# Optimization experiments

Hardware: AMD Instinct MI355X
Metric: run time of the kernel (lower is better)

Reference implementation:

```python
import jax, jax.numpy as jnp
import numpy as np


def setup_inputs() -> dict:
    key = jax.random.key(0)
    ks = jax.random.split(key, 8)
    B, Tq, S, H = 32, 4, 2048, 1024
    return {
        "query": jax.random.normal(ks[0], (B, Tq, H), dtype=jnp.float32),
        "keys": jax.random.normal(ks[1], (S, B, 2 * H), dtype=jnp.float32),
        "Wa_w": jax.random.normal(ks[2], (H, H), dtype=jnp.float32) * 0.02,
        "Wa_b": jax.random.normal(ks[3], (H,), dtype=jnp.float32) * 0.02,
        "Ua_w": jax.random.normal(ks[4], (H, 2 * H), dtype=jnp.float32) * 0.02,
        "Ua_b": jax.random.normal(ks[5], (H,), dtype=jnp.float32) * 0.02,
        "Va_w": jax.random.normal(ks[6], (1, H), dtype=jnp.float32) * 0.02,
        "Va_b": jax.random.normal(ks[7], (1,), dtype=jnp.float32) * 0.02,
    }


def reference(query, keys, Wa_w, Wa_b, Ua_w, Ua_b, Va_w, Va_b):
    # query: [B, Tq, H] -> last step [B, 1, H]
    q = query[:, -1:, :]
    # keys: [S, B, 2H] -> [B, S, 2H]
    k = jnp.transpose(keys, (1, 0, 2))
    # Additive attention scores: Va(tanh(Wa(q) + Ua(k)))
    wq = q @ Wa_w.T + Wa_b                      # [B, 1, H]
    uk = k @ Ua_w.T + Ua_b                      # [B, S, H]
    scores = jnp.tanh(wq + uk) @ Va_w.T + Va_b  # [B, S, 1]
    scores = jnp.transpose(scores, (0, 2, 1))   # [B, 1, S]
    weights = jax.nn.softmax(scores, axis=-1)   # [B, 1, S]
    context = jnp.einsum('bqs,bsd->bqd', weights, k)  # [B, 1, 2H]
    return (context, weights)
```

## Files before the change

kernel.cpp:

```cpp
#include <hip/hip_runtime.h>
#include <hip/hip_bf16.h>

typedef __attribute__((ext_vector_type(4))) float f32x4;
typedef __attribute__((ext_vector_type(8))) short short8;

#define B_   32
#define S_   2048
#define H_   1024
#define D2_  2048
#define BM   256
#define BN   256
#define BK   64
#define NKT  32
#define TILE_SH 16384


__device__ __forceinline__ short f2bf(float f) {
  unsigned u = __float_as_uint(f);
  u = (u + 0x7fffu + ((u >> 16) & 1u)) >> 16;
  return (short)u;
}

__device__ __forceinline__ float bf2f(short s) {
  return __uint_as_float(((unsigned)(unsigned short)s) << 16);
}

__device__ __forceinline__ short8 cvt8(f32x4 a, f32x4 b) {
  short8 o;
  o[0] = f2bf(a.x); o[1] = f2bf(a.y); o[2] = f2bf(a.z); o[3] = f2bf(a.w);
  o[4] = f2bf(b.x); o[5] = f2bf(b.y); o[6] = f2bf(b.z); o[7] = f2bf(b.w);
  return o;
}

__device__ __forceinline__ float fast_tanh(float x) {
  float e = __builtin_amdgcn_exp2f(x * 2.885390081777927f);
  return 1.0f - 2.0f * __builtin_amdgcn_rcpf(e + 1.0f);
}

__device__ __forceinline__ void gload16(const short* g, short* l) {
  __builtin_amdgcn_global_load_lds((const __attribute__((address_space(1))) void*)g,
                                   (__attribute__((address_space(3))) void*)l, 16, 0, 0);
}

__global__ void k_convert_ua(const float* __restrict__ src, short* __restrict__ dst) {
  int idx = blockIdx.x * 256 + threadIdx.x;
  int wu  = idx & 2047;
  int kt  = (idx >> 11) & 31;
  int nt  = idx >> 16;
  int row = wu >> 3;
  int sl  = wu & 7;
  int q   = sl ^ (row & 7);
  const float* s = src + (size_t)(nt * 256 + row) * D2_ + kt * 64 + q * 8;
  f32x4 a = *(const f32x4*)s;
  f32x4 b = *(const f32x4*)(s + 4);
  *(short8*)(dst + (size_t)idx * 8) = cvt8(a, b);
}

__global__ void k_convert_keys(const float* __restrict__ src, short* __restrict__ dst) {
  int idx = blockIdx.x * 256 + threadIdx.x;
  int wu  = idx & 2047;
  int kt  = (idx >> 11) & 31;
  int mt  = idx >> 16;
  int row = wu >> 3;
  int sl  = wu & 7;
  int q   = sl ^ (row & 7);
  const float* s = src + (size_t)(mt * 256 + row) * D2_ + kt * 64 + q * 8;
  f32x4 a = *(const f32x4*)s;
  f32x4 b = *(const f32x4*)(s + 4);
  *(short8*)(dst + (size_t)idx * 8) = cvt8(a, b);
}

__global__ void k_wq(const float* __restrict__ query, const float* __restrict__ Wa_w,
                     const float* __restrict__ Wa_b, const float* __restrict__ Ua_b,
                     float* __restrict__ wqb) {
  int b = blockIdx.x;
  int hc = blockIdx.y;
  int t = threadIdx.x;
  __shared__ float q[H_];
  for (int i = t; i < H_; i += 256) q[i] = query[(size_t)b * (4 * H_) + 3 * H_ + i];
  __syncthreads();
  int h = hc * 128 + (t >> 1);
  int kh = (t & 1) * 512;
  const float* wr = Wa_w + (size_t)h * H_ + kh;
  float acc = 0.f;
  #pragma unroll 8
  for (int k = 0; k < 512; k += 4) {
    f32x4 wv = *(const f32x4*)(wr + k);
    acc += wv.x * q[kh + k] + wv.y * q[kh + k + 1] + wv.z * q[kh + k + 2] + wv.w * q[kh + k + 3];
  }
  acc += __shfl_xor(acc, 1);
  if ((t & 1) == 0) wqb[b * H_ + h] = acc + Wa_b[h] + Ua_b[h];
}

#define AF_READ(mA, mB)                                         \
  af[0] = *(const short8*)&Ac[aread0 + (mA) * 1024];            \
  af[1] = *(const short8*)&Ac[aread1 + (mA) * 1024];            \
  af[2] = *(const short8*)&Ac[aread0 + (mB) * 1024];            \
  af[3] = *(const short8*)&Ac[aread1 + (mB) * 1024];

#define MFMA16(mA, mB)                                                                            \
  __builtin_amdgcn_s_setprio(1);                                                                  \
  _Pragma("unroll")                                                                               \
  for (int n = 0; n < 4; ++n) {                                                                   \
    acc[mA][n] = __builtin_amdgcn_mfma_f32_16x16x32_bf16(af[0], bf[2*n],   acc[mA][n], 0, 0, 0);  \
    acc[mA][n] = __builtin_amdgcn_mfma_f32_16x16x32_bf16(af[1], bf[2*n+1], acc[mA][n], 0, 0, 0);  \
    acc[mB][n] = __builtin_amdgcn_mfma_f32_16x16x32_bf16(af[2], bf[2*n],   acc[mB][n], 0, 0, 0);  \
    acc[mB][n] = __builtin_amdgcn_mfma_f32_16x16x32_bf16(af[3], bf[2*n+1], acc[mB][n], 0, 0, 0);  \
  }                                                                                               \
  __builtin_amdgcn_s_setprio(0);

#define STAGE4(src_, dst_)                         \
  gload16((src_) + 0 * 4096, (dst_) + 0 * 4096 + wu); \
  gload16((src_) + 1 * 4096, (dst_) + 1 * 4096 + wu); \
  gload16((src_) + 2 * 4096, (dst_) + 2 * 4096 + wu); \
  gload16((src_) + 3 * 4096, (dst_) + 3 * 4096 + wu);

__global__ __launch_bounds__(512, 2) void k_gemm_score(
    const short* __restrict__ keys_bf, const short* __restrict__ uab_t,
    const float* __restrict__ wqb, const float* __restrict__ va,
    float* __restrict__ scores_p) {
  __shared__ short As[2][TILE_SH];
  __shared__ short Bs[2][TILE_SH];

  const int bid = blockIdx.x;
  const int g = (bid & 7) * 128 + (bid >> 3);
  const int mt = g >> 2;
  const int nt = g & 3;
  const int r0 = mt * BM;
  const int h0 = nt * BN;

  const int t = threadIdx.x;
  const int lane = t & 63;
  const int w = t >> 6;
  const int wm = w >> 2;
  const int wn = w & 3;

  f32x4 acc[8][4] = {};

  const short* abase = keys_bf + (size_t)mt * (NKT * TILE_SH) + t * 8;
  const short* bbase = uab_t  + (size_t)nt * (NKT * TILE_SH) + t * 8;
  const int wu = w * 512;

  const int lr = lane & 15;
  const int lq = lane >> 4;
  const int sl0 = lq ^ (lr & 7);
  const int aread0 = (wm * 128 + lr) * 64 + sl0 * 8;
  const int aread1 = aread0 ^ 32;
  const int bread0 = (wn * 64 + lr) * 64 + sl0 * 8;
  const int bread1 = bread0 ^ 32;

  {
    STAGE4(abase, &As[0][0])
    STAGE4(bbase, &Bs[0][0])
    asm volatile("s_waitcnt vmcnt(0)" ::: "memory");
    __builtin_amdgcn_s_barrier();
  }

  #pragma unroll 1
  for (int kt = 0; kt < NKT; ++kt) {
    const int cb = kt & 1;
    const bool stage = (kt < NKT - 1);
    const short* Ac = As[cb];
    const short* Bc = Bs[cb];
    const short* anext = abase + (size_t)(kt + 1) * TILE_SH;
    const short* bnext = bbase + (size_t)(kt + 1) * TILE_SH;
    short* Anb = &As[cb ^ 1][0];
    short* Bnb = &Bs[cb ^ 1][0];
    short8 bf[8], af[4];

    #pragma unroll
    for (int n = 0; n < 4; ++n) {
      bf[2 * n]     = *(const short8*)&Bc[bread0 + n * 1024];
      bf[2 * n + 1] = *(const short8*)&Bc[bread1 + n * 1024];
    }
    AF_READ(0, 1)
    if (stage) { STAGE4(anext, Anb) }
    __builtin_amdgcn_s_barrier();
    asm volatile("s_waitcnt lgkmcnt(0)" ::: "memory");
    MFMA16(0, 1)
    __builtin_amdgcn_s_barrier();

    AF_READ(2, 3)
    if (stage) { STAGE4(bnext, Bnb) }
    __builtin_amdgcn_s_barrier();
    asm volatile("s_waitcnt lgkmcnt(0)" ::: "memory");
    MFMA16(2, 3)
    __builtin_amdgcn_s_barrier();

    AF_READ(4, 5)
    __builtin_amdgcn_s_barrier();
    asm volatile("s_waitcnt lgkmcnt(0)" ::: "memory");
    MFMA16(4, 5)
    __builtin_amdgcn_s_barrier();

    AF_READ(6, 7)
    __builtin_amdgcn_s_barrier();
    asm volatile("s_waitcnt lgkmcnt(0)" ::: "memory");
    MFMA16(6, 7)
    asm volatile("s_waitcnt vmcnt(0)" ::: "memory");
    __builtin_amdgcn_s_barrier();
  }

  const int lgrp = lane >> 4;
  const int lc = lane & 15;
  float vah[4];
  #pragma unroll
  for (int n = 0; n < 4; ++n) vah[n] = va[h0 + wn * 64 + n * 16 + lc];
  #pragma unroll
  for (int m = 0; m < 8; ++m) {
    #pragma unroll
    for (int reg = 0; reg < 4; ++reg) {
      int row = wm * 128 + m * 16 + lgrp * 4 + reg;
      int r = r0 + row;
      int bb = r & (B_ - 1);
      const float* wrow = wqb + bb * H_ + h0 + wn * 64 + lc;
      float s = 0.f;
      #pragma unroll
      for (int n = 0; n < 4; ++n)
        s += vah[n] * fast_tanh(acc[m][n][reg] + wrow[n * 16]);
      s += __shfl_xor(s, 1);
      s += __shfl_xor(s, 2);
      s += __shfl_xor(s, 4);
      s += __shfl_xor(s, 8);
      if (lc == 0) scores_p[(size_t)r * 16 + nt * 4 + wn] = s;
    }
  }
}

__global__ __launch_bounds__(512, 2) void k_gemm_rs(
    const float* __restrict__ keys, const short* __restrict__ uab_t,
    const float* __restrict__ wqb, const float* __restrict__ va,
    float* __restrict__ scores_p) {
  __shared__ short As[2][TILE_SH];
  __shared__ short Bs[2][TILE_SH];
  const int bid = blockIdx.x;
  const int g = (bid & 7) * 128 + (bid >> 3);
  const int mt = g >> 2;
  const int nt = g & 3;
  const int r0 = mt * BM;
  const int h0 = nt * BN;
  const int t = threadIdx.x;
  const int lane = t & 63;
  const int w = t >> 6;
  const int wm = w >> 2;
  const int wn = w & 3;
  f32x4 acc[8][4] = {};
  const int arow = t >> 1;
  const int ahalf = t & 1;
  const float* abase = keys + (size_t)(r0 + arow) * D2_ + ahalf * 32;
  int awoff[4];
  #pragma unroll
  for (int j = 0; j < 4; ++j)
    awoff[j] = arow * 64 + ((((ahalf << 2) | j) ^ (arow & 7)) << 3);
  const short* bbase = uab_t + (size_t)nt * NKT * TILE_SH + t * 8;
  const int wu = w * 512;
  const int lr = lane & 15;
  const int lq = lane >> 4;
  const int sl0 = lq ^ (lr & 7);
  const int aread0 = (wm * 128 + lr) * 64 + sl0 * 8;
  const int aread1 = aread0 ^ 32;
  const int bread0 = (wn * 64 + lr) * 64 + sl0 * 8;
  const int bread1 = bread0 ^ 32;
  {
    f32x4 v[8];
    #pragma unroll
    for (int j = 0; j < 8; ++j) v[j] = *(const f32x4*)(abase + j * 4);
    #pragma unroll
    for (int j = 0; j < 4; ++j)
      *(short8*)&As[0][awoff[j]] = cvt8(v[2 * j], v[2 * j + 1]);
    STAGE4(bbase, &Bs[0][0])
    asm volatile("s_waitcnt vmcnt(0) lgkmcnt(0)" ::: "memory");
    __builtin_amdgcn_s_barrier();
  }
  f32x4 av[8];
  #pragma unroll 1
  for (int kt = 0; kt < NKT; ++kt) {
    const int cb = kt & 1;
    const bool stage = (kt < NKT - 1);
    const float* anext = abase + (kt + 1) * BK;
    const short* bnext = bbase + (size_t)(kt + 1) * TILE_SH;
    short* Bnb = &Bs[cb ^ 1][0];
    const short* Ac = As[cb];
    const short* Bc = Bs[cb];
    short8 bf[8], af[4];
    #pragma unroll
    for (int n = 0; n < 4; ++n) {
      bf[2 * n]     = *(const short8*)&Bc[bread0 + n * 1024];
      bf[2 * n + 1] = *(const short8*)&Bc[bread1 + n * 1024];
    }
    AF_READ(0, 1)
    if (stage) {
      #pragma unroll
      for (int j = 0; j < 8; ++j) av[j] = *(const f32x4*)(anext + j * 4);
    }
    __builtin_amdgcn_s_barrier();
    asm volatile("s_waitcnt lgkmcnt(0)" ::: "memory");
    MFMA16(0, 1)
    __builtin_amdgcn_s_barrier();
    AF_READ(2, 3)
    if (stage) {
      gload16(bnext + 0 * 4096, Bnb + 0 * 4096 + wu);
      gload16(bnext + 1 * 4096, Bnb + 1 * 4096 + wu);
    }
    __builtin_amdgcn_s_barrier();
    asm volatile("s_waitcnt lgkmcnt(0)" ::: "memory");
    MFMA16(2, 3)
    __builtin_amdgcn_s_barrier();
    AF_READ(4, 5)
    if (stage) {
      gload16(bnext + 2 * 4096, Bnb + 2 * 4096 + wu);
      gload16(bnext + 3 * 4096, Bnb + 3 * 4096 + wu);
    }
    __builtin_amdgcn_s_barrier();
    asm volatile("s_waitcnt lgkmcnt(0)" ::: "memory");
    MFMA16(4, 5)
    __builtin_amdgcn_s_barrier();
    AF_READ(6, 7)
    if (stage) {
      #pragma unroll
      for (int j = 0; j < 4; ++j)
        *(short8*)&As[cb ^ 1][awoff[j]] = cvt8(av[2 * j], av[2 * j + 1]);
    }
    __builtin_amdgcn_s_barrier();
    asm volatile("s_waitcnt lgkmcnt(0)" ::: "memory");
    MFMA16(6, 7)
    asm volatile("s_waitcnt vmcnt(0) lgkmcnt(0)" ::: "memory");
    __builtin_amdgcn_s_barrier();
  }
  const int lgrp = lane >> 4;
  const int lc = lane & 15;
  float vah[4];
  #pragma unroll
  for (int n = 0; n < 4; ++n) vah[n] = va[h0 + wn * 64 + n * 16 + lc];
  #pragma unroll
  for (int m = 0; m < 8; ++m) {
    #pragma unroll
    for (int reg = 0; reg < 4; ++reg) {
      int row = wm * 128 + m * 16 + lgrp * 4 + reg;
      int r = r0 + row;
      int bb = r & (B_ - 1);
      const float* wrow = wqb + bb * H_ + h0 + wn * 64 + lc;
      float s = 0.f;
      #pragma unroll
      for (int n = 0; n < 4; ++n)
        s += vah[n] * fast_tanh(acc[m][n][reg] + wrow[n * 16]);
      s += __shfl_xor(s, 1);
      s += __shfl_xor(s, 2);
      s += __shfl_xor(s, 4);
      s += __shfl_xor(s, 8);
      if (lc == 0) scores_p[(size_t)r * 16 + nt * 4 + wn] = s;
    }
  }
}

__global__ void k_softmax(const float* __restrict__ scores_p, float* __restrict__ out) {
  int b = blockIdx.x;
  int t = threadIdx.x;
  __shared__ float sc[S_];
  __shared__ float red[4];
  float lmax = -3.4e38f;
  #pragma unroll
  for (int i = 0; i < 8; ++i) {
    int s = t + i * 256;
    const float* p = scores_p + ((size_t)s * B_ + b) * 16;
    f32x4 p0 = *(const f32x4*)p;
    f32x4 p1 = *(const f32x4*)(p + 4);
    f32x4 p2 = *(const f32x4*)(p + 8);
    f32x4 p3 = *(const f32x4*)(p + 12);
    f32x4 ps = p0 + p1 + p2 + p3;
    float v = ps.x + ps.y + ps.z + ps.w;
    sc[s] = v;
    lmax = fmaxf(lmax, v);
  }
  #pragma unroll
  for (int o = 32; o >= 1; o >>= 1) lmax = fmaxf(lmax, __shfl_xor(lmax, o));
  if ((t & 63) == 0) red[t >> 6] = lmax;
  __syncthreads();
  float gmax = fmaxf(fmaxf(red[0], red[1]), fmaxf(red[2], red[3]));
  __syncthreads();
  float lsum = 0.f;
  #pragma unroll
  for (int i = 0; i < 8; ++i) {
    int s = t + i * 256;
    float e = __builtin_amdgcn_exp2f((sc[s] - gmax) * 1.4426950408889634f);
    sc[s] = e;
    lsum += e;
  }
  #pragma unroll
  for (int o = 32; o >= 1; o >>= 1) lsum += __shfl_xor(lsum, o);
  if ((t & 63) == 0) red[t >> 6] = lsum;
  __syncthreads();
  float inv = 1.0f / (red[0] + red[1] + red[2] + red[3]);
  for (int i = 0; i < 8; ++i) {
    int s = t + i * 256;
    out[(size_t)65536 + b * S_ + s] = sc[s] * inv;
  }
}

__global__ __launch_bounds__(256) void k_ctx_partial_bf2(const short* __restrict__ keys_bf,
                                                         const float* __restrict__ wts,
                                                         float* __restrict__ cp) {
  const int kt = blockIdx.x;
  const int mtc = blockIdx.y;
  const int t = threadIdx.x;
  const int cg = t >> 5;
  const int b = t & 31;
  const int slot = cg ^ (b & 7);
  const float* wbase = wts + (size_t)b * S_ + mtc * 128;
  f32x4 accA = {}, accB = {};
  #pragma unroll 2
  for (int c = 0; c < 16; ++c) {
    const short* tb = keys_bf + ((size_t)((mtc * 16 + c) * 32 + kt)) * TILE_SH + (slot << 3);
    f32x4 w0 = *(const f32x4*)(wbase + c * 8);
    f32x4 w1 = *(const f32x4*)(wbase + c * 8 + 4);
    float wg[8] = {w0.x, w0.y, w0.z, w0.w, w1.x, w1.y, w1.z, w1.w};
    #pragma unroll
    for (int s8 = 0; s8 < 8; ++s8) {
      short8 v = *(const short8*)(tb + (s8 * 32 + b) * 64);
      float wgt = wg[s8];
      accA.x += wgt * bf2f(v[0]); accA.y += wgt * bf2f(v[1]);
      accA.z += wgt * bf2f(v[2]); accA.w += wgt * bf2f(v[3]);
      accB.x += wgt * bf2f(v[4]); accB.y += wgt * bf2f(v[5]);
      accB.z += wgt * bf2f(v[6]); accB.w += wgt * bf2f(v[7]);
    }
  }
  float* o = cp + ((size_t)mtc * B_ + b) * D2_ + kt * 64 + cg * 8;
  *(f32x4*)o = accA;
  *(f32x4*)(o + 4) = accB;
}

__global__ void k_ctx_partial(const float* __restrict__ keys, const float* __restrict__ wts,
                              float* __restrict__ cp) {
  int b = blockIdx.x;
  int dc = blockIdx.y;
  int scn = blockIdx.z;
  int t = threadIdx.x;
  __shared__ float wl[256];
  int s0 = scn * 256;
  wl[t] = wts[b * S_ + s0 + t];
  __syncthreads();
  int d = dc * 1024 + t * 4;
  f32x4 acc = {};
  #pragma unroll 4
  for (int i = 0; i < 256; ++i) {
    int s = s0 + i;
    f32x4 kv = *(const f32x4*)(keys + ((size_t)s * B_ + b) * D2_ + d);
    acc += kv * wl[i];
  }
  *(f32x4*)(cp + ((size_t)scn * B_ + b) * D2_ + d) = acc;
}

__global__ void k_ctx_reduce(const float* __restrict__ cp, float* __restrict__ out, int np) {
  int i = blockIdx.x * 256 + threadIdx.x;
  float s = 0.f;
  for (int j = 0; j < np; ++j) s += cp[(size_t)j * 65536 + i];
  out[i] = s;
}

extern "C" void kernel_launch(void* const* d_in, const int* in_sizes, int n_in,
                              void* d_out, int out_size, void* d_ws, size_t ws_size,
                              hipStream_t stream) {
  const float* query = (const float*)d_in[0];
  const float* keys  = (const float*)d_in[1];
  const float* Wa_w  = (const float*)d_in[2];
  const float* Wa_b  = (const float*)d_in[3];
  const float* Ua_w  = (const float*)d_in[4];
  const float* Ua_b  = (const float*)d_in[5];
  const float* Va_w  = (const float*)d_in[6];
  float* out = (float*)d_out;
  char* ws = (char*)d_ws;

  const size_t KEYS_BF_BYTES = 268435456ull;
  const size_t TAIL = 16ull * 1024 * 1024;
  bool big = ws_size >= KEYS_BF_BYTES + TAIL;

  if (big) {
    short* keys_bf = (short*)ws;
    char* base = ws + KEYS_BF_BYTES;
    short* uab_t = (short*)(base);
    float* wqb = (float*)(base + 4u * 1024 * 1024);
    float* sp  = (float*)(base + 4u * 1024 * 1024 + 128 * 1024);
    float* cp  = (float*)(base + 8u * 1024 * 1024 + 256 * 1024);

    hipLaunchKernelGGL(k_convert_ua, dim3(1024), dim3(256), 0, stream, Ua_w, uab_t);
    hipLaunchKernelGGL(k_convert_keys, dim3(65536), dim3(256), 0, stream, keys, keys_bf);
    hipLaunchKernelGGL(k_wq, dim3(32, 8), dim3(256), 0, stream, query, Wa_w, Wa_b, Ua_b, wqb);
    hipLaunchKernelGGL(k_gemm_score, dim3(1024), dim3(512), 0, stream, keys_bf, uab_t, wqb, Va_w, sp);
    hipLaunchKernelGGL(k_softmax, dim3(32), dim3(256), 0, stream, sp, out);
    hipLaunchKernelGGL(k_ctx_partial_bf2, dim3(32, 16), dim3(256), 0, stream, keys_bf, out + 65536, cp);
    hipLaunchKernelGGL(k_ctx_reduce, dim3(256), dim3(256), 0, stream, cp, out, 16);
  } else {
    short* uab_t = (short*)(ws);
    float* wqb = (float*)(ws + 4u * 1024 * 1024);
    float* sp  = (float*)(ws + 4u * 1024 * 1024 + 128 * 1024);
    float* cp  = (float*)(ws + 8u * 1024 * 1024 + 256 * 1024);

    hipLaunchKernelGGL(k_convert_ua, dim3(1024), dim3(256), 0, stream, Ua_w, uab_t);
    hipLaunchKernelGGL(k_wq, dim3(32, 8), dim3(256), 0, stream, query, Wa_w, Wa_b, Ua_b, wqb);
    hipLaunchKernelGGL(k_gemm_rs, dim3(1024), dim3(512), 0, stream, keys, uab_t, wqb, Va_w, sp);
    hipLaunchKernelGGL(k_softmax, dim3(32), dim3(256), 0, stream, sp, out);
    hipLaunchKernelGGL(k_ctx_partial, dim3(32, 2, 8), dim3(256), 0, stream, keys, out + 65536, cp);
    hipLaunchKernelGGL(k_ctx_reduce, dim3(256), dim3(256), 0, stream, cp, out, 8);
  }
}
```

Baseline: 507.8 us.

## Halve GEMM K-tile to 32 and cut per-iteration barriers in score kernels

Shrinks the GEMM K tile from 64 to 32, doubling the K iterations. The pre-swizzled bf16 layouts in the convert kernels and the context kernel are rewritten to match the new 32-wide tiles. The main loop now loads all A/B fragments up front and uses partial lgkmcnt waits with sched_barrier, issuing MFMAs in two groups and replacing about eight barriers per iteration with one or two. The aim is to cut synchronization overhead and shared-memory footprint, possibly raising occupancy. The cost is more loop iterations, with less MFMA work available to hide global-load latency in each one.

```diff
diff --git a/kernel.cpp b/kernel.cpp
--- a/kernel.cpp
+++ b/kernel.cpp
@@ -10,9 +10,9 @@
 #define D2_  2048
 #define BM   256
 #define BN   256
-#define BK   64
-#define NKT  32
-#define TILE_SH 16384
+#define BK   32
+#define NKT  64
+#define TILE_SH 8192
 
 
 __device__ __forceinline__ short f2bf(float f) {
@@ -44,13 +44,13 @@
 
 __global__ void k_convert_ua(const float* __restrict__ src, short* __restrict__ dst) {
   int idx = blockIdx.x * 256 + threadIdx.x;
-  int wu  = idx & 2047;
-  int kt  = (idx >> 11) & 31;
-  int nt  = idx >> 16;
-  int row = wu >> 3;
-  int sl  = wu & 7;
-  int q   = sl ^ (row & 7);
-  const float* s = src + (size_t)(nt * 256 + row) * D2_ + kt * 64 + q * 8;
+  int unit = idx & 1023;
+  int kts  = (idx >> 10) & 63;
+  int nt   = idx >> 16;
+  int row  = unit >> 2;
+  int sl   = unit & 3;
+  int q    = sl ^ (row & 3);
+  const float* s = src + (size_t)(nt * 256 + row) * D2_ + kts * 32 + q * 8;
   f32x4 a = *(const f32x4*)s;
   f32x4 b = *(const f32x4*)(s + 4);
   *(short8*)(dst + (size_t)idx * 8) = cvt8(a, b);
@@ -58,13 +58,13 @@
 
 __global__ void k_convert_keys(const float* __restrict__ src, short* __restrict__ dst) {
   int idx = blockIdx.x * 256 + threadIdx.x;
-  int wu  = idx & 2047;
-  int kt  = (idx >> 11) & 31;
-  int mt  = idx >> 16;
-  int row = wu >> 3;
-  int sl  = wu & 7;
-  int q   = sl ^ (row & 7);
-  const float* s = src + (size_t)(mt * 256 + row) * D2_ + kt * 64 + q * 8;
+  int unit = idx & 1023;
+  int kts  = (idx >> 10) & 63;
+  int mt   = idx >> 16;
+  int row  = unit >> 2;
+  int sl   = unit & 3;
+  int q    = sl ^ (row & 3);
+  const float* s = src + (size_t)(mt * 256 + row) * D2_ + kts * 32 + q * 8;
   f32x4 a = *(const f32x4*)s;
   f32x4 b = *(const f32x4*)(s + 4);
   *(short8*)(dst + (size_t)idx * 8) = cvt8(a, b);
@@ -92,28 +92,16 @@
   if ((t & 1) == 0) wqb[b * H_ + h] = acc + Wa_b[h] + Ua_b[h];
 }
 
-#define AF_READ(mA, mB)                                         \
-  af[0] = *(const short8*)&Ac[aread0 + (mA) * 1024];            \
-  af[1] = *(const short8*)&Ac[aread1 + (mA) * 1024];            \
-  af[2] = *(const short8*)&Ac[aread0 + (mB) * 1024];            \
-  af[3] = *(const short8*)&Ac[aread1 + (mB) * 1024];
-
-#define MFMA16(mA, mB)                                                                            \
+#define MCL16(mb, AF)                                                                             \
   __builtin_amdgcn_s_setprio(1);                                                                  \
   _Pragma("unroll")                                                                               \
   for (int n = 0; n < 4; ++n) {                                                                   \
-    acc[mA][n] = __builtin_amdgcn_mfma_f32_16x16x32_bf16(af[0], bf[2*n],   acc[mA][n], 0, 0, 0);  \
-    acc[mA][n] = __builtin_amdgcn_mfma_f32_16x16x32_bf16(af[1], bf[2*n+1], acc[mA][n], 0, 0, 0);  \
-    acc[mB][n] = __builtin_amdgcn_mfma_f32_16x16x32_bf16(af[2], bf[2*n],   acc[mB][n], 0, 0, 0);  \
-    acc[mB][n] = __builtin_amdgcn_mfma_f32_16x16x32_bf16(af[3], bf[2*n+1], acc[mB][n], 0, 0, 0);  \
+    _Pragma("unroll")                                                                             \
+    for (int i = 0; i < 4; ++i)                                                                   \
+      acc[(mb) + i][n] =                                                                          \
+          __builtin_amdgcn_mfma_f32_16x16x32_bf16(AF[i], bf[n], acc[(mb) + i][n], 0, 0, 0);       \
   }                                                                                               \
   __builtin_amdgcn_s_setprio(0);
-
-#define STAGE4(src_, dst_)                         \
-  gload16((src_) + 0 * 4096, (dst_) + 0 * 4096 + wu); \
-  gload16((src_) + 1 * 4096, (dst_) + 1 * 4096 + wu); \
-  gload16((src_) + 2 * 4096, (dst_) + 2 * 4096 + wu); \
-  gload16((src_) + 3 * 4096, (dst_) + 3 * 4096 + wu);
 
 __global__ __launch_bounds__(512, 2) void k_gemm_score(
     const short* __restrict__ keys_bf, const short* __restrict__ uab_t,
@@ -143,60 +131,50 @@
 
   const int lr = lane & 15;
   const int lq = lane >> 4;
-  const int sl0 = lq ^ (lr & 7);
-  const int aread0 = (wm * 128 + lr) * 64 + sl0 * 8;
-  const int aread1 = aread0 ^ 32;
-  const int bread0 = (wn * 64 + lr) * 64 + sl0 * 8;
-  const int bread1 = bread0 ^ 32;
+  const int slot = lq ^ (lr & 3);
+  const int aoff = (wm * 128 + lr) * 32 + slot * 8;
+  const int boff = (wn * 64 + lr) * 32 + slot * 8;
 
   {
-    STAGE4(abase, &As[0][0])
-    STAGE4(bbase, &Bs[0][0])
+    gload16(abase,        &As[0][wu]);
+    gload16(abase + 4096, &As[0][4096 + wu]);
+    gload16(bbase,        &Bs[0][wu]);
+    gload16(bbase + 4096, &Bs[0][4096 + wu]);
     asm volatile("s_waitcnt vmcnt(0)" ::: "memory");
     __builtin_amdgcn_s_barrier();
   }
 
+  short8 bf[4], af0[4], af1[4];
+
   #pragma unroll 1
-  for (int kt = 0; kt < NKT; ++kt) {
-    const int cb = kt & 1;
-    const bool stage = (kt < NKT - 1);
+  for (int kts = 0; kts < NKT; ++kts) {
+    const int cb = kts & 1;
+    const bool stage = (kts < NKT - 1);
     const short* Ac = As[cb];
     const short* Bc = Bs[cb];
-    const short* anext = abase + (size_t)(kt + 1) * TILE_SH;
-    const short* bnext = bbase + (size_t)(kt + 1) * TILE_SH;
     short* Anb = &As[cb ^ 1][0];
     short* Bnb = &Bs[cb ^ 1][0];
-    short8 bf[8], af[4];
-
-    #pragma unroll
-    for (int n = 0; n < 4; ++n) {
-      bf[2 * n]     = *(const short8*)&Bc[bread0 + n * 1024];
-      bf[2 * n + 1] = *(const short8*)&Bc[bread1 + n * 1024];
-    }
-    AF_READ(0, 1)
-    if (stage) { STAGE4(anext, Anb) }
-    __builtin_amdgcn_s_barrier();
+    const short* anext = abase + (size_t)(kts + 1) * TILE_SH;
+    const short* bnext = bbase + (size_t)(kts + 1) * TILE_SH;
+
+    #pragma unroll
+    for (int n = 0; n < 4; ++n) bf[n] = *(const short8*)&Bc[boff + n * 512];
+    #pragma unroll
+    for (int i = 0; i < 4; ++i) af0[i] = *(const short8*)&Ac[aoff + i * 512];
+    #pragma unroll
+    for (int i = 0; i < 4; ++i) af1[i] = *(const short8*)&Ac[aoff + (4 + i) * 512];
+    if (stage) {
+      gload16(anext,        Anb + wu);
+      gload16(anext + 4096, Anb + 4096 + wu);
+      gload16(bnext,        Bnb + wu);
+      gload16(bnext + 4096, Bnb + 4096 + wu);
+    }
+    asm volatile("s_waitcnt lgkmcnt(4)" ::: "memory");
+    __builtin_amdgcn_sched_barrier(0);
+    MCL16(0, af0)
     asm volatile("s_waitcnt lgkmcnt(0)" ::: "memory");
-    MFMA16(0, 1)
-    __builtin_amdgcn_s_barrier();
-
-    AF_READ(2, 3)
-    if (stage) { STAGE4(bnext, Bnb) }
-    __builtin_amdgcn_s_barrier();
-    asm volatile("s_waitcnt lgkmcnt(0)" ::: "memory");
-    MFMA16(2, 3)
-    __builtin_amdgcn_s_barrier();
-
-    AF_READ(4, 5)
-    __builtin_amdgcn_s_barrier();
-    asm volatile("s_waitcnt lgkmcnt(0)" ::: "memory");
-    MFMA16(4, 5)
-    __builtin_amdgcn_s_barrier();
-
-    AF_READ(6, 7)
-    __builtin_amdgcn_s_barrier();
-    asm volatile("s_waitcnt lgkmcnt(0)" ::: "memory");
-    MFMA16(6, 7)
+    __builtin_amdgcn_sched_barrier(0);
+    MCL16(4, af1)
     asm volatile("s_waitcnt vmcnt(0)" ::: "memory");
     __builtin_amdgcn_s_barrier();
   }
@@ -246,84 +224,69 @@
   const int wn = w & 3;
   f32x4 acc[8][4] = {};
   const int arow = t >> 1;
-  const int ahalf = t & 1;
-  const float* abase = keys + (size_t)(r0 + arow) * D2_ + ahalf * 32;
-  int awoff[4];
-  #pragma unroll
-  for (int j = 0; j < 4; ++j)
-    awoff[j] = arow * 64 + ((((ahalf << 2) | j) ^ (arow & 7)) << 3);
+  const int hh = t & 1;
+  const float* abase = keys + (size_t)(r0 + arow) * D2_ + hh * 16;
+  int awoff[2];
+  #pragma unroll
+  for (int j = 0; j < 2; ++j)
+    awoff[j] = arow * 32 + (((2 * hh + j) ^ (arow & 3)) << 3);
   const short* bbase = uab_t + (size_t)nt * NKT * TILE_SH + t * 8;
   const int wu = w * 512;
   const int lr = lane & 15;
   const int lq = lane >> 4;
-  const int sl0 = lq ^ (lr & 7);
-  const int aread0 = (wm * 128 + lr) * 64 + sl0 * 8;
-  const int aread1 = aread0 ^ 32;
-  const int bread0 = (wn * 64 + lr) * 64 + sl0 * 8;
-  const int bread1 = bread0 ^ 32;
+  const int slot = lq ^ (lr & 3);
+  const int aoff = (wm * 128 + lr) * 32 + slot * 8;
+  const int boff = (wn * 64 + lr) * 32 + slot * 8;
+  short8 bf[4], af0[4], af1[4];
   {
-    f32x4 v[8];
-    #pragma unroll
-    for (int j = 0; j < 8; ++j) v[j] = *(const f32x4*)(abase + j * 4);
-    #pragma unroll
-    for (int j = 0; j < 4; ++j)
-      *(short8*)&As[0][awoff[j]] = cvt8(v[2 * j], v[2 * j + 1]);
-    STAGE4(bbase, &Bs[0][0])
+    f32x4 v0 = *(const f32x4*)(abase);
+    f32x4 v1 = *(const f32x4*)(abase + 4);
+    f32x4 v2 = *(const f32x4*)(abase + 8);
+    f32x4 v3 = *(const f32x4*)(abase + 12);
+    *(short8*)&As[0][awoff[0]] = cvt8(v0, v1);
+    *(short8*)&As[0][awoff[1]] = cvt8(v2, v3);
+    gload16(bbase,        &Bs[0][wu]);
+    gload16(bbase + 4096, &Bs[0][4096 + wu]);
     asm volatile("s_waitcnt vmcnt(0) lgkmcnt(0)" ::: "memory");
     __builtin_amdgcn_s_barrier();
   }
-  f32x4 av[8];
   #pragma unroll 1
-  for (int kt = 0; kt < NKT; ++kt) {
-    const int cb = kt & 1;
-    const bool stage = (kt < NKT - 1);
-    const float* anext = abase + (kt + 1) * BK;
-    const short* bnext = bbase + (size_t)(kt + 1) * TILE_SH;
+  for (int kts = 0; kts < NKT; ++kts) {
+    const int cb = kts & 1;
+    const bool stage = (kts < NKT - 1);
+    const float* anext = abase + (kts + 1) * BK;
+    const short* bnext = bbase + (size_t)(kts + 1) * TILE_SH;
+    short* Anb = &As[cb ^ 1][0];
     short* Bnb = &Bs[cb ^ 1][0];
     const short* Ac = As[cb];
     const short* Bc = Bs[cb];
-    short8 bf[8], af[4];
-    #pragma unroll
-    for (int n = 0; n < 4; ++n) {
-      bf[2 * n]     = *(const short8*)&Bc[bread0 + n * 1024];
-      bf[2 * n + 1] = *(const short8*)&Bc[bread1 + n * 1024];
-    }
-    AF_READ(0, 1)
+
+    #pragma unroll
+    for (int n = 0; n < 4; ++n) bf[n] = *(const short8*)&Bc[boff + n * 512];
+    #pragma unroll
+    for (int i = 0; i < 4; ++i) af0[i] = *(const short8*)&Ac[aoff + i * 512];
+    #pragma unroll
+    for (int i = 0; i < 4; ++i) af1[i] = *(const short8*)&Ac[aoff + (4 + i) * 512];
+    f32x4 v0, v1, v2, v3;
     if (stage) {
-      #pragma unroll
-      for (int j = 0; j < 8; ++j) av[j] = *(const f32x4*)(anext + j * 4);
-    }
+      v0 = *(const f32x4*)(anext);
+      v1 = *(const f32x4*)(anext + 4);
+      v2 = *(const f32x4*)(anext + 8);
+      v3 = *(const f32x4*)(anext + 12);
+      gload16(bnext,        Bnb + wu);
+      gload16(bnext + 4096, Bnb + 4096 + wu);
+    }
+    asm volatile("s_waitcnt lgkmcnt(4)" ::: "memory");
+    __builtin_amdgcn_sched_barrier(0);
+    MCL16(0, af0)
+    asm volatile("s_waitcnt lgkmcnt(0)" ::: "memory");
+    __builtin_amdgcn_sched_barrier(0);
+    MCL16(4, af1)
     __builtin_amdgcn_s_barrier();
-    asm volatile("s_waitcnt lgkmcnt(0)" ::: "memory");
-    MFMA16(0, 1)
-    __builtin_amdgcn_s_barrier();
-    AF_READ(2, 3)
     if (stage) {
-      gload16(bnext + 0 * 4096, Bnb + 0 * 4096 + wu);
-      gload16(bnext + 1 * 4096, Bnb + 1 * 4096 + wu);
-    }
-    __builtin_amdgcn_s_barrier();
-    asm volatile("s_waitcnt lgkmcnt(0)" ::: "memory");
-    MFMA16(2, 3)
-    __builtin_amdgcn_s_barrier();
-    AF_READ(4, 5)
-    if (stage) {
-      gload16(bnext + 2 * 4096, Bnb + 2 * 4096 + wu);
-      gload16(bnext + 3 * 4096, Bnb + 3 * 4096 + wu);
-    }
-    __builtin_amdgcn_s_barrier();
-    asm volatile("s_waitcnt lgkmcnt(0)" ::: "memory");
-    MFMA16(4, 5)
-    __builtin_amdgcn_s_barrier();
-    AF_READ(6, 7)
-    if (stage) {
-      #pragma unroll
-      for (int j = 0; j < 4; ++j)
-        *(short8*)&As[cb ^ 1][awoff[j]] = cvt8(av[2 * j], av[2 * j + 1]);
-    }
-    __builtin_amdgcn_s_barrier();
-    asm volatile("s_waitcnt lgkmcnt(0)" ::: "memory");
-    MFMA16(6, 7)
+      *(short8*)&Anb[awoff[0]] = cvt8(v0, v1);
+      *(short8*)&Anb[awoff[1]] = cvt8(v2, v3);
+    }
     asm volatile("s_waitcnt vmcnt(0) lgkmcnt(0)" ::: "memory");
     __builtin_amdgcn_s_barrier();
   }
@@ -400,23 +363,24 @@
 __global__ __launch_bounds__(256) void k_ctx_partial_bf2(const short* __restrict__ keys_bf,
                                                          const float* __restrict__ wts,
                                                          float* __restrict__ cp) {
-  const int kt = blockIdx.x;
+  const int ktp = blockIdx.x;
   const int mtc = blockIdx.y;
   const int t = threadIdx.x;
   const int cg = t >> 5;
   const int b = t & 31;
-  const int slot = cg ^ (b & 7);
+  const int kts = ktp * 2 + (cg >> 2);
+  const int slot = (cg & 3) ^ (b & 3);
   const float* wbase = wts + (size_t)b * S_ + mtc * 128;
   f32x4 accA = {}, accB = {};
   #pragma unroll 2
   for (int c = 0; c < 16; ++c) {
-    const short* tb = keys_bf + ((size_t)((mtc * 16 + c) * 32 + kt)) * TILE_SH + (slot << 3);
+    const short* tb = keys_bf + ((size_t)((mtc * 16 + c) * 64 + kts)) * TILE_SH + (slot << 3);
     f32x4 w0 = *(const f32x4*)(wbase + c * 8);
     f32x4 w1 = *(const f32x4*)(wbase + c * 8 + 4);
     float wg[8] = {w0.x, w0.y, w0.z, w0.w, w1.x, w1.y, w1.z, w1.w};
     #pragma unroll
     for (int s8 = 0; s8 < 8; ++s8) {
-      short8 v = *(const short8*)(tb + (s8 * 32 + b) * 64);
+      short8 v = *(const short8*)(tb + (s8 * 32 + b) * 32);
       float wgt = wg[s8];
       accA.x += wgt * bf2f(v[0]); accA.y += wgt * bf2f(v[1]);
       accA.z += wgt * bf2f(v[2]); accA.w += wgt * bf2f(v[3]);
@@ -424,7 +388,7 @@
       accB.z += wgt * bf2f(v[6]); accB.w += wgt * bf2f(v[7]);
     }
   }
-  float* o = cp + ((size_t)mtc * B_ + b) * D2_ + kt * 64 + cg * 8;
+  float* o = cp + ((size_t)mtc * B_ + b) * D2_ + ktp * 64 + cg * 8;
   *(f32x4*)o = accA;
   *(f32x4*)(o + 4) = accB;
 }
```

Measured after the change: 523.0 us. 3.0% more time.
